# Performance work log

Hardware: AMD Instinct MI355X
Metric: run time of the kernel (lower is better)

## Reference

```python
import jax, jax.numpy as jnp
import numpy as np

S, T, V = 1024, 8192, 64  # states, time steps, output alphabet


def setup_inputs() -> dict:
    key = jax.random.key(0)
    k1, k2, k3, k4 = jax.random.split(key, 4)
    sequence = jax.random.randint(k1, (T,), 0, V, dtype=jnp.int32)
    # Scaled so the multiplicative alpha recurrence stays O(1) over T steps
    initial = jax.random.uniform(k2, (S, 1), dtype=jnp.float32) / S
    transfer = jax.random.uniform(k3, (S, S), dtype=jnp.float32) * (2.0 / S)
    emission = jax.random.uniform(k4, (S, V), dtype=jnp.float32) * 2.0
    return {"sequence": sequence, "initial": initial,
            "transfer": transfer, "emission": emission}


def reference(sequence, initial, transfer, emission):
    """HMM forward (alpha) recurrence.

    Original numpy loop:
      alpha[:, t] = sum_i alpha[i, t-1] * transfer[i, j] * emission[j, seq[t-1]]
    i.e. a_t = (a_{t-1} @ A) * B[:, obs_t], expressed as a lax.scan.
    Returns alpha with shape (S, T+1), matching the original.
    """
    em_t = emission[:, sequence].T  # (T, S): em_t[t, j] = B[j, obs_t]

    def step(a, e):
        a_new = (a @ transfer) * e  # fused matvec + elementwise
        return a_new, a_new

    a0 = initial[:, 0]  # (S,)
    _, alphas = jax.lax.scan(step, a0, em_t)  # (T, S)
    alpha = jnp.concatenate([a0[None, :], alphas], axis=0).T  # (S, T+1)
    return alpha
```

## Files before the change

### kernel.cpp

```cpp
#include <hip/hip_runtime.h>


typedef _Float16 half8 __attribute__((ext_vector_type(8)));
typedef float f32x4 __attribute__((ext_vector_type(4)));

#define SD 1024
#define TD 8192
#define VD 64
#define RCH 2048
#define LST 6

__device__ __forceinline__ half8 u2h(uint4 u) { return __builtin_bit_cast(half8, u); }

__global__ void pack_f16(const float* __restrict__ A, _Float16* __restrict__ BH)
{
    int kt = blockIdx.x;
    int ct = blockIdx.y;
    int l  = threadIdx.x;
    half8 vh;
    #pragma unroll
    for (int j = 0; j < 8; ++j) {
        int k = kt * 32 + (l >> 4) * 8 + j;
        int n = ct * 16 + (l & 15);
        vh[j] = (_Float16)(A[(size_t)k * SD + n] * 1024.0f);
    }
    *(half8*)(BH + ((size_t)(kt * 64 + ct) * 64 + l) * 8) = vh;
}

__global__ void et_f(const float* __restrict__ E, float* __restrict__ Et)
{
    int v = blockIdx.x;
    for (int j = threadIdx.x; j < SD; j += 256)
        Et[v * SD + j] = E[(size_t)j * VD + v] * (1.0f / 1024.0f);
}

__global__ void init_cur(const float* __restrict__ initial, _Float16* __restrict__ CH)
{
    int g  = blockIdx.x >> 5;
    int kc = blockIdx.x & 31;
    int l  = threadIdx.x;
    int R  = g * 16 + (l & 15);
    bool ex = (R == 0);
    half8 vh;
    #pragma unroll
    for (int j = 0; j < 8; ++j) {
        int C = kc * 32 + (l >> 4) * 8 + j;
        float v = ex ? initial[C] * 2048.0f : 1.0f;
        vh[j] = (_Float16)v;
    }
    ((half8*)CH)[(size_t)(g * 32 + kc) * 64 + l] = vh;
}

__global__ __launch_bounds__(256, 2) void hmm_step(
    const _Float16* __restrict__ CHin, _Float16* __restrict__ CHout,
    const _Float16* __restrict__ BH, const float* __restrict__ Et,
    const int* __restrict__ seq, float* __restrict__ aw, float* __restrict__ alpha,
    double* __restrict__ sigS, double* __restrict__ sigE, int s)
{
    __shared__ __align__(16) _Float16 sB[64 * 512];
    __shared__ int sObs[128];

    const int tid = threadIdx.x;
    const int l   = tid & 63;
    const int w   = tid >> 6;
    const int mt  = blockIdx.x;
    const int nt  = blockIdx.y;

    if (tid < 128) {
        int R = mt * 128 + tid;
        int t = 4 * R + s - 1;
        sObs[tid] = (t >= 1) ? seq[t - 1] : -1;
    }

    const uint4* BH4 = (const uint4*)BH;
    uint4* sB4 = (uint4*)sB;
    #pragma unroll
    for (int i = 0; i < 16; ++i) {
        int q  = i * 256 + tid;
        int fl = q >> 6, li = q & 63;
        int kt = fl >> 1, ctl = fl & 1;
        sB4[q] = BH4[(size_t)((kt * 64 + nt * 2 + ctl) * 64 + li)];
    }
    __syncthreads();

    f32x4 acc[2][2];
    #pragma unroll
    for (int rt = 0; rt < 2; ++rt)
        #pragma unroll
        for (int ct = 0; ct < 2; ++ct)
            #pragma unroll
            for (int i = 0; i < 4; ++i) acc[rt][ct][i] = 0.0f;

    const uint4* CH4 = (const uint4*)CHin;
    const int g0 = mt * 8 + w * 2;

    #pragma unroll 4
    for (int kt = 0; kt < 32; ++kt) {
        half8 a0 = u2h(CH4[(size_t)(g0 * 32 + kt) * 64 + l]);
        half8 a1 = u2h(CH4[(size_t)((g0 + 1) * 32 + kt) * 64 + l]);
        half8 b0 = *(const half8*)&sB[((kt * 2 + 0) * 64 + l) * 8];
        half8 b1 = *(const half8*)&sB[((kt * 2 + 1) * 64 + l) * 8];
        acc[0][0] = __builtin_amdgcn_mfma_f32_16x16x32_f16(a0, b0, acc[0][0], 0, 0, 0);
        acc[0][1] = __builtin_amdgcn_mfma_f32_16x16x32_f16(a0, b1, acc[0][1], 0, 0, 0);
        acc[1][0] = __builtin_amdgcn_mfma_f32_16x16x32_f16(a1, b0, acc[1][0], 0, 0, 0);
        acc[1][1] = __builtin_amdgcn_mfma_f32_16x16x32_f16(a1, b1, acc[1][1], 0, 0, 0);
    }
    __syncthreads();

    const bool red   = (s == 1) || (s == LST - 1);
    const bool store = (s >= 2);
    const bool wback = (s < LST - 1);
    double* sig = (s == 1) ? sigS : sigE;
    _Float16* tS = sB;

    #pragma unroll
    for (int rt = 0; rt < 2; ++rt) {
        #pragma unroll
        for (int i = 0; i < 4; ++i) {
            int rl  = w * 32 + rt * 16 + (l >> 4) * 4 + i;
            int R   = mt * 128 + rl;
            int t   = 4 * R + s - 1;
            int obs = sObs[rl];
            float rs = 0.0f;
            #pragma unroll
            for (int ct = 0; ct < 2; ++ct) {
                int col = nt * 32 + ct * 16 + (l & 15);
                float v;
                if (obs >= 0) {
                    v = acc[rt][ct][i] * Et[obs * SD + col];
                } else {
                    int gg = R >> 4, mm = R & 15, wi = col & 31;
                    size_t idx = ((size_t)(gg * 32 + nt) * 64 + (mm + (wi >> 3) * 16)) * 8 + (wi & 7);
                    v = (float)CHin[idx];
                }
                if (wback) {
                    int gl = rl >> 4;
                    int wi = col & 31;
                    int lp = (rl & 15) + (wi >> 3) * 16;
                    tS[(gl * 64 + lp) * 8 + (wi & 7)] = (_Float16)v;
                }
                if (store) {
                    if (aw) aw[(size_t)t * SD + col] = v;
                    else    alpha[(size_t)col * (TD + 1) + t] = v;
                }
                rs += v;
            }
            if (red) {
                rs += __shfl_xor(rs, 1);
                rs += __shfl_xor(rs, 2);
                rs += __shfl_xor(rs, 4);
                rs += __shfl_xor(rs, 8);
                if ((l & 15) == 0) atomicAdd(&sig[R], (double)rs);
            }
        }
    }
    if (wback) {
        __syncthreads();
        const uint4* tS4 = (const uint4*)tS;
        #pragma unroll
        for (int i = 0; i < 2; ++i) {
            int q  = i * 256 + tid;
            int gl = q >> 6, li = q & 63;
            ((uint4*)CHout)[(size_t)((mt * 8 + gl) * 32 + nt) * 64 + li] = tS4[q];
        }
    }
}

__global__ void hmm_scan3(const double* __restrict__ ss, const double* __restrict__ se,
                          float* __restrict__ scale)
{
    __shared__ double tp[256];
    int tid = threadIdx.x;
    double q[RCH / 256];
    double local = 1.0;
    #pragma unroll
    for (int u = 0; u < RCH / 256; ++u) {
        int k = tid * (RCH / 256) + u;
        double qq = (k == 0) ? (1.0 / 2048.0) : (se[k - 1] / ss[k]);
        q[u] = qq;
        local *= qq;
    }
    double x = local;
    tp[tid] = x;
    __syncthreads();
    for (int off = 1; off < 256; off <<= 1) {
        double y = (tid >= off) ? tp[tid - off] : 1.0;
        __syncthreads();
        x *= y;
        tp[tid] = x;
        __syncthreads();
    }
    double run = (tid > 0) ? tp[tid - 1] : 1.0;
    #pragma unroll
    for (int u = 0; u < RCH / 256; ++u) {
        run *= q[u];
        scale[tid * (RCH / 256) + u] = (float)run;
    }
}

__global__ void hmm_applyA(const float* __restrict__ initial,
                           const float* __restrict__ scale,
                           const float* __restrict__ aw,
                           float* __restrict__ alpha)
{
    __shared__ float tile[64][65];
    int jt = blockIdx.x;
    int tt = blockIdx.y;
    int tid = threadIdx.x;
    int lane = tid & 63, q = tid >> 6;
    int t0 = tt * 64, j0 = jt * 64;

    #pragma unroll
    for (int i = 0; i < 16; ++i) {
        int t = t0 + q * 16 + i;
        int j = j0 + lane;
        float v = 0.0f;
        if (t == 0)       v = initial[j];
        else if (t <= TD) v = aw[(size_t)t * SD + j] * scale[(t - 1) >> 2];
        tile[q * 16 + i][lane] = v;
    }
    __syncthreads();
    #pragma unroll
    for (int i = 0; i < 16; ++i) {
        int j = j0 + q * 16 + i;
        int t = t0 + lane;
        if (t <= TD) alpha[(size_t)j * (TD + 1) + t] = tile[lane][q * 16 + i];
    }
}

__global__ void hmm_applyB(const float* __restrict__ initial,
                           const float* __restrict__ scale,
                           float* __restrict__ alpha)
{
    __shared__ float sc[RCH];
    int tid = threadIdx.x;
    for (int k = tid; k < RCH; k += 256) sc[k] = scale[k];
    __syncthreads();
    int srow = blockIdx.x;
    float* row = alpha + (size_t)srow * (TD + 1);
    if (tid == 0) row[0] = initial[srow];
    for (int t = 1 + tid; t <= TD; t += 256) row[t] *= sc[(t - 1) >> 2];
}

__global__ __launch_bounds__(512) void hmm_chunks_fb(
    const int* __restrict__ seq, const float* __restrict__ initial,
    const float* __restrict__ A, const float* __restrict__ E,
    float* __restrict__ alpha, float* __restrict__ sig_start, float* __restrict__ sig_end)
{
    __shared__ __align__(16) float cur[8][SD];
    __shared__ float wred[8][8];
    const int tid = threadIdx.x;
    const int lane = tid & 63;
    const int wav = tid >> 6;
    const int j0 = tid * 2;
    const int b = blockIdx.x;
    const float2* __restrict__ A2 = (const float2*)A;

    for (int r = 0; r < 8; ++r) {
        int k = b * 8 + r;
        bool exact = (k * 4 - 6) <= 0;
        for (int j = tid; j < SD; j += 512) cur[r][j] = exact ? initial[j] : 1.0f;
    }
    __syncthreads();

    for (int s = 0; s < 10; ++s) {
        float acc[8][2];
        #pragma unroll
        for (int r = 0; r < 8; ++r) { acc[r][0] = 0.0f; acc[r][1] = 0.0f; }
        float2 a0 = A2[0 * (SD / 2) + tid];
        float2 a1 = A2[1 * (SD / 2) + tid];
        float2 a2 = A2[2 * (SD / 2) + tid];
        float2 a3 = A2[3 * (SD / 2) + tid];
        for (int i4 = 0; i4 < SD / 4; ++i4) {
            int ni = ((i4 + 1) & (SD / 4 - 1)) * 4;
            float2 b0 = A2[(ni + 0) * (SD / 2) + tid];
            float2 b1 = A2[(ni + 1) * (SD / 2) + tid];
            float2 b2 = A2[(ni + 2) * (SD / 2) + tid];
            float2 b3 = A2[(ni + 3) * (SD / 2) + tid];
            int i = i4 * 4;
            #pragma unroll
            for (int r = 0; r < 8; ++r) {
                float4 cc = *(const float4*)&cur[r][i];
                acc[r][0] = fmaf(cc.x, a0.x, acc[r][0]);
                acc[r][1] = fmaf(cc.x, a0.y, acc[r][1]);
                acc[r][0] = fmaf(cc.y, a1.x, acc[r][0]);
                acc[r][1] = fmaf(cc.y, a1.y, acc[r][1]);
                acc[r][0] = fmaf(cc.z, a2.x, acc[r][0]);
                acc[r][1] = fmaf(cc.z, a2.y, acc[r][1]);
                acc[r][0] = fmaf(cc.w, a3.x, acc[r][0]);
                acc[r][1] = fmaf(cc.w, a3.y, acc[r][1]);
            }
            a0 = b0; a1 = b1; a2 = b2; a3 = b3;
        }
        __syncthreads();
        #pragma unroll
        for (int r = 0; r < 8; ++r) {
            int k = b * 8 + r;
            int t = k * 4 - 6 + 1 + s;
            if (t >= 1) {
                int obs = seq[t - 1];
                float e0 = E[(j0 + 0) * VD + obs];
                float e1 = E[(j0 + 1) * VD + obs];
                float v0 = acc[r][0] * e0;
                float v1 = acc[r][1] * e1;
                cur[r][j0 + 0] = v0;
                cur[r][j0 + 1] = v1;
                if (s >= 6) {
                    alpha[(size_t)(j0 + 0) * (TD + 1) + t] = v0;
                    alpha[(size_t)(j0 + 1) * (TD + 1) + t] = v1;
                }
            }
        }
        __syncthreads();
        if (s == 5 || s == 9) {
            #pragma unroll
            for (int r = 0; r < 8; ++r) {
                float p = cur[r][j0] + cur[r][j0 + 1];
                for (int off = 32; off > 0; off >>= 1) p += __shfl_down(p, off, 64);
                if (lane == 0) wred[r][wav] = p;
            }
            __syncthreads();
            if (tid < 8) {
                float tot = 0.0f;
                #pragma unroll
                for (int wv = 0; wv < 8; ++wv) tot += wred[tid][wv];
                int k = b * 8 + tid;
                if (s == 5) sig_start[k] = tot; else sig_end[k] = tot;
            }
            __syncthreads();
        }
    }
}

__global__ void hmm_scan_fb(const float* __restrict__ sig_start,
                            const float* __restrict__ sig_end,
                            float* __restrict__ scale)
{
    __shared__ float tp[256];
    int tid = threadIdx.x;
    float q[8];
    float local = 1.0f;
    #pragma unroll
    for (int u = 0; u < 8; ++u) {
        int k = tid * 8 + u;
        float qq = (k == 0) ? 1.0f : (sig_end[k - 1] / sig_start[k]);
        q[u] = qq;
        local *= qq;
    }
    float x = local;
    tp[tid] = x;
    __syncthreads();
    for (int off = 1; off < 256; off <<= 1) {
        float y = (tid >= off) ? tp[tid - off] : 1.0f;
        __syncthreads();
        x *= y;
        tp[tid] = x;
        __syncthreads();
    }
    float run = (tid > 0) ? tp[tid - 1] : 1.0f;
    #pragma unroll
    for (int u = 0; u < 8; ++u) {
        run *= q[u];
        scale[tid * 8 + u] = run;
    }
}

__global__ void hmm_apply_fb(const float* __restrict__ initial,
                             const float* __restrict__ scale,
                             float* __restrict__ alpha)
{
    __shared__ float sc[2048];
    int tid = threadIdx.x;
    for (int k = tid; k < 2048; k += 256) sc[k] = scale[k];
    __syncthreads();
    int srow = blockIdx.x;
    float* row = alpha + (size_t)srow * (TD + 1);
    if (tid == 0) row[0] = initial[srow];
    for (int t = 1 + tid; t <= TD; t += 256) row[t] *= sc[(t - 1) >> 2];
}

extern "C" void kernel_launch(void* const* d_in, const int* in_sizes, int n_in,
                              void* d_out, int out_size, void* d_ws, size_t ws_size,
                              hipStream_t stream)
{
    const int*   seq     = (const int*)d_in[0];
    const float* initial = (const float*)d_in[1];
    const float* A       = (const float*)d_in[2];
    const float* E       = (const float*)d_in[3];
    float* alpha = (float*)d_out;
    char* w = (char*)d_ws;

    const size_t offBH  = 0;
    const size_t offEt  = 2097152;
    const size_t offC   = 2097152 + 262144;
    const size_t offSig = offC + 2 * 4194304;
    const size_t offAw  = offSig + 40960;
    const size_t needMid  = offAw;
    const size_t needFull = offAw + (size_t)(TD + 1) * SD * 4;

    if (ws_size >= needMid) {
        _Float16* BH  = (_Float16*)(w + offBH);
        float*    Et  = (float*)(w + offEt);
        _Float16* CA  = (_Float16*)(w + offC);
        _Float16* CB  = (_Float16*)(w + offC + 4194304);
        double* sigS  = (double*)(w + offSig);
        double* sigE  = (double*)(w + offSig + 16384);
        float*  scale = (float*)(w + offSig + 32768);
        float*  aw    = (ws_size >= needFull) ? (float*)(w + offAw) : nullptr;

        hipLaunchKernelGGL(pack_f16, dim3(32, 64), dim3(64), 0, stream, A, BH);
        hipLaunchKernelGGL(et_f, dim3(64), dim3(256), 0, stream, E, Et);
        hipLaunchKernelGGL(init_cur, dim3(4096), dim3(64), 0, stream, initial, CA);
        hipMemsetAsync(w + offSig, 0, 32768, stream);

        _Float16* buf[2] = {CA, CB};
        for (int s = 0; s < LST; ++s) {
            hipLaunchKernelGGL(hmm_step, dim3(16, 32), dim3(256), 0, stream,
                               buf[s & 1], buf[(s + 1) & 1], BH, Et, seq,
                               aw, alpha, sigS, sigE, s);
        }
        hipLaunchKernelGGL(hmm_scan3, dim3(1), dim3(256), 0, stream, sigS, sigE, scale);
        if (aw) hipLaunchKernelGGL(hmm_applyA, dim3(16, 129), dim3(256), 0, stream,
                                   initial, scale, aw, alpha);
        else    hipLaunchKernelGGL(hmm_applyB, dim3(SD), dim3(256), 0, stream,
                                   initial, scale, alpha);
    } else {
        float* ws = (float*)d_ws;
        float* sig_start = ws;
        float* sig_end   = ws + 2048;
        float* scale     = ws + 4096;
        hipLaunchKernelGGL(hmm_chunks_fb, dim3(256), dim3(512), 0, stream,
                           seq, initial, A, E, alpha, sig_start, sig_end);
        hipLaunchKernelGGL(hmm_scan_fb, dim3(1), dim3(256), 0, stream,
                           sig_start, sig_end, scale);
        hipLaunchKernelGGL(hmm_apply_fb, dim3(SD), dim3(256), 0, stream,
                           initial, scale, alpha);
    }
}
```

Baseline: 191.1 us.

## Merge prep kernels and read transfer operand directly from global in step kernel

Fuses the three preprocessing kernels (f16 packing of the transfer matrix, emission transpose, initial state packing) into one launch with block-range dispatch, removing two launch overheads. In hmm_step, the 64 KB shared-memory staging of the B tile is removed; B fragments are loaded directly from global memory in the MFMA loop, shared memory shrinks to an 8 KB epilogue tile, and launch bounds are raised to 4 blocks per CU for higher occupancy. This trades reuse through LDS for repeated global/L2 reads of B across waves.

Result: slower. 200.5 us (+4.9%).

```diff
diff --git a/kernel.cpp b/kernel.cpp
--- a/kernel.cpp
+++ b/kernel.cpp
@@ -12,52 +12,54 @@
 
 __device__ __forceinline__ half8 u2h(uint4 u) { return __builtin_bit_cast(half8, u); }
 
-__global__ void pack_f16(const float* __restrict__ A, _Float16* __restrict__ BH)
-{
-    int kt = blockIdx.x;
-    int ct = blockIdx.y;
-    int l  = threadIdx.x;
-    half8 vh;
-    #pragma unroll
-    for (int j = 0; j < 8; ++j) {
-        int k = kt * 32 + (l >> 4) * 8 + j;
-        int n = ct * 16 + (l & 15);
-        vh[j] = (_Float16)(A[(size_t)k * SD + n] * 1024.0f);
-    }
-    *(half8*)(BH + ((size_t)(kt * 64 + ct) * 64 + l) * 8) = vh;
-}
-
-__global__ void et_f(const float* __restrict__ E, float* __restrict__ Et)
-{
-    int v = blockIdx.x;
-    for (int j = threadIdx.x; j < SD; j += 256)
-        Et[v * SD + j] = E[(size_t)j * VD + v] * (1.0f / 1024.0f);
-}
-
-__global__ void init_cur(const float* __restrict__ initial, _Float16* __restrict__ CH)
-{
-    int g  = blockIdx.x >> 5;
-    int kc = blockIdx.x & 31;
-    int l  = threadIdx.x;
-    int R  = g * 16 + (l & 15);
-    bool ex = (R == 0);
-    half8 vh;
-    #pragma unroll
-    for (int j = 0; j < 8; ++j) {
-        int C = kc * 32 + (l >> 4) * 8 + j;
-        float v = ex ? initial[C] * 2048.0f : 1.0f;
-        vh[j] = (_Float16)v;
-    }
-    ((half8*)CH)[(size_t)(g * 32 + kc) * 64 + l] = vh;
-}
-
-__global__ __launch_bounds__(256, 2) void hmm_step(
+__global__ __launch_bounds__(256) void hmm_prep(
+    const float* __restrict__ A, const float* __restrict__ E,
+    const float* __restrict__ initial,
+    _Float16* __restrict__ BH, float* __restrict__ Et, _Float16* __restrict__ CH)
+{
+    const int b = blockIdx.x;
+    const int tid = threadIdx.x;
+    if (b < 512) {
+        int pair = b * 4 + (tid >> 6);
+        int kt = pair >> 6, ct = pair & 63;
+        int l  = tid & 63;
+        half8 vh;
+        #pragma unroll
+        for (int j = 0; j < 8; ++j) {
+            int k = kt * 32 + (l >> 4) * 8 + j;
+            int n = ct * 16 + (l & 15);
+            vh[j] = (_Float16)(A[(size_t)k * SD + n] * 1024.0f);
+        }
+        *(half8*)(BH + ((size_t)pair * 64 + l) * 8) = vh;
+    } else if (b < 576) {
+        int v = b - 512;
+        for (int j = tid; j < SD; j += 256)
+            Et[v * SD + j] = E[(size_t)j * VD + v] * (1.0f / 1024.0f);
+    } else {
+        int ob = (b - 576) * 4 + (tid >> 6);
+        int g  = ob >> 5;
+        int kc = ob & 31;
+        int l  = tid & 63;
+        int R  = g * 16 + (l & 15);
+        bool ex = (R == 0);
+        half8 vh;
+        #pragma unroll
+        for (int j = 0; j < 8; ++j) {
+            int C = kc * 32 + (l >> 4) * 8 + j;
+            float v = ex ? initial[C] * 2048.0f : 1.0f;
+            vh[j] = (_Float16)v;
+        }
+        ((half8*)CH)[(size_t)(g * 32 + kc) * 64 + l] = vh;
+    }
+}
+
+__global__ __launch_bounds__(256, 4) void hmm_step(
     const _Float16* __restrict__ CHin, _Float16* __restrict__ CHout,
     const _Float16* __restrict__ BH, const float* __restrict__ Et,
     const int* __restrict__ seq, float* __restrict__ aw, float* __restrict__ alpha,
     double* __restrict__ sigS, double* __restrict__ sigE, int s)
 {
-    __shared__ __align__(16) _Float16 sB[64 * 512];
+    __shared__ __align__(16) _Float16 tS[4096];
     __shared__ int sObs[128];
 
     const int tid = threadIdx.x;
@@ -71,16 +73,6 @@
         int t = 4 * R + s - 1;
         sObs[tid] = (t >= 1) ? seq[t - 1] : -1;
     }
-
-    const uint4* BH4 = (const uint4*)BH;
-    uint4* sB4 = (uint4*)sB;
-    #pragma unroll
-    for (int i = 0; i < 16; ++i) {
-        int q  = i * 256 + tid;
-        int fl = q >> 6, li = q & 63;
-        int kt = fl >> 1, ctl = fl & 1;
-        sB4[q] = BH4[(size_t)((kt * 64 + nt * 2 + ctl) * 64 + li)];
-    }
     __syncthreads();
 
     f32x4 acc[2][2];
@@ -92,26 +84,25 @@
             for (int i = 0; i < 4; ++i) acc[rt][ct][i] = 0.0f;
 
     const uint4* CH4 = (const uint4*)CHin;
+    const uint4* BH4 = (const uint4*)BH;
     const int g0 = mt * 8 + w * 2;
 
     #pragma unroll 4
     for (int kt = 0; kt < 32; ++kt) {
         half8 a0 = u2h(CH4[(size_t)(g0 * 32 + kt) * 64 + l]);
         half8 a1 = u2h(CH4[(size_t)((g0 + 1) * 32 + kt) * 64 + l]);
-        half8 b0 = *(const half8*)&sB[((kt * 2 + 0) * 64 + l) * 8];
-        half8 b1 = *(const half8*)&sB[((kt * 2 + 1) * 64 + l) * 8];
+        half8 b0 = u2h(BH4[(size_t)((kt * 64 + nt * 2 + 0) * 64 + l)]);
+        half8 b1 = u2h(BH4[(size_t)((kt * 64 + nt * 2 + 1) * 64 + l)]);
         acc[0][0] = __builtin_amdgcn_mfma_f32_16x16x32_f16(a0, b0, acc[0][0], 0, 0, 0);
         acc[0][1] = __builtin_amdgcn_mfma_f32_16x16x32_f16(a0, b1, acc[0][1], 0, 0, 0);
         acc[1][0] = __builtin_amdgcn_mfma_f32_16x16x32_f16(a1, b0, acc[1][0], 0, 0, 0);
         acc[1][1] = __builtin_amdgcn_mfma_f32_16x16x32_f16(a1, b1, acc[1][1], 0, 0, 0);
     }
-    __syncthreads();
 
     const bool red   = (s == 1) || (s == LST - 1);
     const bool store = (s >= 2);
     const bool wback = (s < LST - 1);
     double* sig = (s == 1) ? sigS : sigE;
-    _Float16* tS = sB;
 
     #pragma unroll
     for (int rt = 0; rt < 2; ++rt) {
@@ -408,9 +399,8 @@
         float*  scale = (float*)(w + offSig + 32768);
         float*  aw    = (ws_size >= needFull) ? (float*)(w + offAw) : nullptr;
 
-        hipLaunchKernelGGL(pack_f16, dim3(32, 64), dim3(64), 0, stream, A, BH);
-        hipLaunchKernelGGL(et_f, dim3(64), dim3(256), 0, stream, E, Et);
-        hipLaunchKernelGGL(init_cur, dim3(4096), dim3(64), 0, stream, initial, CA);
+        hipLaunchKernelGGL(hmm_prep, dim3(1600), dim3(256), 0, stream,
+                           A, E, initial, BH, Et, CA);
         hipMemsetAsync(w + offSig, 0, 32768, stream);
 
         _Float16* buf[2] = {CA, CB};
```
